# Kernel tuning notes

Hardware: AMD Instinct MI355X
Metric: run time of the kernel (lower is better)

Reference implementation:

```python
import jax, jax.numpy as jnp
import numpy as np

B, LQ, LK = 8, 256, 256
Q_SIZE = K_SIZE = H = D_V = 256
MASK_VALUE = -1000000.0


def setup_inputs() -> dict:
    key = jax.random.key(0)
    kq, kk, kv, kl, kwq, kwk, kwv = jax.random.split(key, 7)
    # Linear weights, torch nn.Linear stores (out, in); init ~ U(-1/sqrt(in), 1/sqrt(in))
    def lin(k, out_f, in_f):
        bound = 1.0 / np.sqrt(in_f)
        return jax.random.uniform(k, (out_f, in_f), jnp.float32, -bound, bound)
    return {
        "queries": jax.random.normal(kq, (B, LQ, Q_SIZE), jnp.float32),
        "keyes": jax.random.normal(kk, (B, LK, K_SIZE), jnp.float32),
        "values": jax.random.normal(kv, (B, LK, D_V), jnp.float32),
        "valid_lens": jax.random.randint(kl, (B,), 1, LK + 1),
        "W_q": lin(kwq, H, Q_SIZE),
        "W_k": lin(kwk, H, K_SIZE),
        "W_v": lin(kwv, 1, H),
    }


def reference(queries, keyes, values, valid_lens, W_q, W_k, W_v):
    # Projections (nn.Linear without bias): x @ W.T
    q = jnp.einsum("bqd,hd->bqh", queries, W_q)            # (B, Lq, H)
    k = jnp.einsum("bkd,hd->bkh", keyes, W_k)              # (B, Lk, H)
    # Broadcast-add + tanh: (B, Lq, Lk, H)
    features = jnp.tanh(q[:, :, None, :] + k[:, None, :, :])
    # W_v reduction H -> 1, squeeze: scores (B, Lq, Lk)
    scores = jnp.einsum("bqkh,h->bqk", features, W_v[0])
    # sequence_mask over the last (key) axis with value -1e6
    lk = scores.shape[-1]
    mask = jnp.arange(lk)[None, None, :] < valid_lens[:, None, None]  # (B,1,Lk)
    scores = jnp.where(mask, scores, MASK_VALUE)
    # NOTE: this repo's masked_softmax normalizes over dim=1 (the query axis),
    # faithfully reproduced here.
    attention_weights = jax.nn.softmax(scores, axis=1)
    # dropout is identity in eval / p=0.0
    return jnp.einsum("bqk,bkd->bqd", attention_weights, values)
```

## Files before the change

### kernel.cpp

```cpp
#include <hip/hip_runtime.h>

typedef float vf4 __attribute__((ext_vector_type(4)));

#define LOG2E 1.4426950408889634f
#define TWO_LOG2E 2.8853900817779268f

__device__ __forceinline__ float fexp2(float x) { return __builtin_amdgcn_exp2f(x); }
__device__ __forceinline__ float frcp(float x) { return __builtin_amdgcn_rcpf(x); }

__global__ __launch_bounds__(256) void proj_kernel(
    const float* __restrict__ queries, const float* __restrict__ keyes,
    const float* __restrict__ Wq, const float* __restrict__ Wk,
    float* __restrict__ Qp, float* __restrict__ Kp) {
  __shared__ alignas(16) float At[16 * 68];
  __shared__ alignas(16) float Bt[16 * 68];
  const int t = threadIdx.x;
  const int m0 = blockIdx.x * 64;
  const int n0 = blockIdx.y * 64;
  const bool isQ = (m0 < 2048);
  const float* X = isQ ? queries : keyes;
  const float* W = isQ ? Wq : Wk;
  float* C = isQ ? Qp : Kp;
  const int mb = isQ ? m0 : (m0 - 2048);

  const int lm = t >> 2;
  const int lq = t & 3;
  const int mm4 = (t & 15) * 4;
  const int nn4 = (t >> 4) * 4;

  float acc[4][4] = {};
  for (int kc = 0; kc < 256; kc += 16) {
    __syncthreads();
    vf4 xa = *(const vf4*)&X[(mb + lm) * 256 + kc + lq * 4];
    vf4 wb = *(const vf4*)&W[(n0 + lm) * 256 + kc + lq * 4];
#pragma unroll
    for (int c = 0; c < 4; ++c) {
      At[(lq * 4 + c) * 68 + lm] = xa[c];
      Bt[(lq * 4 + c) * 68 + lm] = wb[c];
    }
    __syncthreads();
#pragma unroll
    for (int kk = 0; kk < 16; ++kk) {
      vf4 a4 = *(const vf4*)&At[kk * 68 + mm4];
      vf4 b4 = *(const vf4*)&Bt[kk * 68 + nn4];
#pragma unroll
      for (int i = 0; i < 4; ++i)
#pragma unroll
        for (int j = 0; j < 4; ++j) acc[i][j] += a4[i] * b4[j];
    }
  }
#pragma unroll
  for (int i = 0; i < 4; ++i) {
    vf4 o = {acc[i][0] * TWO_LOG2E, acc[i][1] * TWO_LOG2E,
             acc[i][2] * TWO_LOG2E, acc[i][3] * TWO_LOG2E};
    *(vf4*)&C[(mb + mm4 + i) * 256 + n0 + nn4] = o;
  }
}

__global__ __launch_bounds__(256) void scores_exp_kernel(
    const float* __restrict__ Qp, const float* __restrict__ Kp,
    const float* __restrict__ Wv, const int* __restrict__ valid_lens,
    float* __restrict__ E) {
  __shared__ alignas(16) float Qs[32 * 32];
  __shared__ alignas(16) float Ks[32 * 32];
  __shared__ alignas(16) float wvs[256];
  const int t = threadIdx.x;
  const int i0 = blockIdx.x * 32;
  const int j0 = blockIdx.y * 32;
  const int b = blockIdx.z;
  const int ti = t & 15;
  const int tj = t >> 4;

  float Swv;
  {
    vf4 w4 = *(const vf4*)&Wv[(t & 63) * 4];
    float sw = w4[0] + w4[1] + w4[2] + w4[3];
#pragma unroll
    for (int off = 1; off < 64; off <<= 1) sw += __shfl_xor(sw, off, 64);
    Swv = sw;
  }
  if (t < 64) *(vf4*)&wvs[t * 4] = *(const vf4*)&Wv[t * 4];

  const int srow = t >> 3;
  const int scg = t & 7;
  const int swcol = ((scg ^ (srow & 7)) << 2);
  const int qxor = ti & 7;
  const int kxor = tj & 7;

  float acc[2][2] = {};
  for (int hc = 0; hc < 8; ++hc) {
    __syncthreads();
    vf4 qv = *(const vf4*)&Qp[(((b << 8) + i0 + srow) << 8) + hc * 32 + scg * 4];
    vf4 kv = *(const vf4*)&Kp[(((b << 8) + j0 + srow) << 8) + hc * 32 + scg * 4];
    *(vf4*)&Qs[srow * 32 + swcol] = qv;
    *(vf4*)&Ks[srow * 32 + swcol] = kv;
    __syncthreads();
#pragma unroll
    for (int hh = 0; hh < 8; ++hh) {
      vf4 q0 = *(const vf4*)&Qs[ti * 32 + ((hh ^ qxor) << 2)];
      vf4 q1 = *(const vf4*)&Qs[(ti + 16) * 32 + ((hh ^ qxor) << 2)];
      vf4 k0 = *(const vf4*)&Ks[tj * 32 + ((hh ^ kxor) << 2)];
      vf4 k1 = *(const vf4*)&Ks[(tj + 16) * 32 + ((hh ^ kxor) << 2)];
      vf4 wv4 = *(const vf4*)&wvs[hc * 32 + hh * 4];
#pragma unroll
      for (int e = 0; e < 4; ++e) {
        const float we = wv4[e];
        acc[0][0] += we * frcp(fexp2(q0[e] + k0[e]) + 1.0f);
        acc[0][1] += we * frcp(fexp2(q0[e] + k1[e]) + 1.0f);
        acc[1][0] += we * frcp(fexp2(q1[e] + k0[e]) + 1.0f);
        acc[1][1] += we * frcp(fexp2(q1[e] + k1[e]) + 1.0f);
      }
    }
  }

  const int len = valid_lens[b];
#pragma unroll
  for (int c = 0; c < 2; ++c) {
    const int j = j0 + tj + 16 * c;
    const bool masked = (j >= len);
#pragma unroll
    for (int r = 0; r < 2; ++r) {
      const int i = i0 + ti + 16 * r;
      const float score = Swv - 2.0f * acc[r][c];
      const float ev = masked ? 1.0f : fexp2(score * LOG2E);
      E[(((b << 8) + j) << 8) + i] = ev;
    }
  }
}

__global__ __launch_bounds__(256) void rowsum_kernel(
    const float* __restrict__ E, float* __restrict__ R) {
  const int t = threadIdx.x;
  const int l = t & 63;
  const int row = blockIdx.x * 4 + (t >> 6);
  vf4 v = *(const vf4*)&E[(row << 8) + l * 4];
  float s = v[0] + v[1] + v[2] + v[3];
#pragma unroll
  for (int off = 1; off < 64; off <<= 1) s += __shfl_xor(s, off, 64);
  if (l == 0) R[row] = frcp(s);
}

__global__ __launch_bounds__(128) void out_kernel(
    const float* __restrict__ E, const float* __restrict__ R,
    const float* __restrict__ V, float* __restrict__ out) {
  __shared__ alignas(16) float As[32 * 36];
  __shared__ alignas(16) float Bs[32 * 68];
  const int t = threadIdx.x;
  const int i0 = blockIdx.x * 32;
  const int d0 = blockIdx.y * 64;
  const int b = blockIdx.z;
  const int ti = t & 7;
  const int td = t >> 3;
  const int srow = t >> 2;
  const int scg = t & 3;

  float acc[4][4] = {};
  for (int jc = 0; jc < 8; ++jc) {
    const int jb = jc * 32;
    __syncthreads();
    const float rj = R[(b << 8) + jb + srow];
#pragma unroll
    for (int s = 0; s < 2; ++s) {
      const int col = scg * 8 + s * 4;
      vf4 a = *(const vf4*)&E[(((b << 8) + jb + srow) << 8) + i0 + col];
      *(vf4*)&As[srow * 36 + col] = a * rj;
    }
#pragma unroll
    for (int s = 0; s < 4; ++s) {
      const int col = scg * 16 + s * 4;
      *(vf4*)&Bs[srow * 68 + col] =
          *(const vf4*)&V[(((b << 8) + jb + srow) << 8) + d0 + col];
    }
    __syncthreads();
#pragma unroll
    for (int j = 0; j < 32; ++j) {
      vf4 a4 = *(const vf4*)&As[j * 36 + ti * 4];
      vf4 b4 = *(const vf4*)&Bs[j * 68 + td * 4];
#pragma unroll
      for (int r = 0; r < 4; ++r)
#pragma unroll
        for (int c = 0; c < 4; ++c) acc[r][c] += a4[r] * b4[c];
    }
  }
#pragma unroll
  for (int r = 0; r < 4; ++r) {
    vf4 o = {acc[r][0], acc[r][1], acc[r][2], acc[r][3]};
    *(vf4*)&out[(((b << 8) + i0 + ti * 4 + r) << 8) + d0 + td * 4] = o;
  }
}

extern "C" void kernel_launch(void* const* d_in, const int* in_sizes, int n_in,
                              void* d_out, int out_size, void* d_ws, size_t ws_size,
                              hipStream_t stream) {
  const float* queries = (const float*)d_in[0];
  const float* keyes = (const float*)d_in[1];
  const float* values = (const float*)d_in[2];
  const int* valid_lens = (const int*)d_in[3];
  const float* Wq = (const float*)d_in[4];
  const float* Wk = (const float*)d_in[5];
  const float* Wv = (const float*)d_in[6];
  float* out = (float*)d_out;

  float* Qp = (float*)d_ws;
  float* Kp = Qp + 524288;
  float* E = Kp + 524288;
  float* R = E + 524288;

  proj_kernel<<<dim3(64, 4), 256, 0, stream>>>(queries, keyes, Wq, Wk, Qp, Kp);
  scores_exp_kernel<<<dim3(8, 8, 8), 256, 0, stream>>>(Qp, Kp, Wv, valid_lens, E);
  rowsum_kernel<<<512, 256, 0, stream>>>(E, R);
  out_kernel<<<dim3(8, 4, 8), 128, 0, stream>>>(E, R, values, out);
}
```

Measured before the change: 129.7 us.

## Split-K projection and fuse softmax row sums into score kernel via atomics

The projection GEMM is split along K into two halves written to separate buffers, which doubles its block count; the score kernel sums the two halves when it loads them. The separate rowsum kernel is removed. Per-key row sums are reduced with shuffles in the score kernel and accumulated with atomicAdd into a buffer that the projection kernel zeroes. This saves one launch and one full pass over E, at the cost of twice the Q/K projection traffic, extra atomics, and a nondeterministic summation order.

New measurement: 125.4 us. 3.3% less time.

```diff
diff --git a/kernel.cpp b/kernel.cpp
--- a/kernel.cpp
+++ b/kernel.cpp
@@ -11,16 +11,22 @@
 __global__ __launch_bounds__(256) void proj_kernel(
     const float* __restrict__ queries, const float* __restrict__ keyes,
     const float* __restrict__ Wq, const float* __restrict__ Wk,
-    float* __restrict__ Qp, float* __restrict__ Kp) {
+    float* __restrict__ QpH, float* __restrict__ KpH,
+    float* __restrict__ Rsum) {
   __shared__ alignas(16) float At[16 * 68];
   __shared__ alignas(16) float Bt[16 * 68];
   const int t = threadIdx.x;
+  if (blockIdx.x == 0 && blockIdx.y == 0 && blockIdx.z == 0) {
+    *(vf4*)&Rsum[t * 8] = (vf4){0.f, 0.f, 0.f, 0.f};
+    *(vf4*)&Rsum[t * 8 + 4] = (vf4){0.f, 0.f, 0.f, 0.f};
+  }
   const int m0 = blockIdx.x * 64;
   const int n0 = blockIdx.y * 64;
+  const int k0 = blockIdx.z * 128;
   const bool isQ = (m0 < 2048);
   const float* X = isQ ? queries : keyes;
   const float* W = isQ ? Wq : Wk;
-  float* C = isQ ? Qp : Kp;
+  float* C = (isQ ? QpH : KpH) + blockIdx.z * 524288;
   const int mb = isQ ? m0 : (m0 - 2048);
 
   const int lm = t >> 2;
@@ -29,7 +35,7 @@
   const int nn4 = (t >> 4) * 4;
 
   float acc[4][4] = {};
-  for (int kc = 0; kc < 256; kc += 16) {
+  for (int kc = k0; kc < k0 + 128; kc += 16) {
     __syncthreads();
     vf4 xa = *(const vf4*)&X[(mb + lm) * 256 + kc + lq * 4];
     vf4 wb = *(const vf4*)&W[(n0 + lm) * 256 + kc + lq * 4];
@@ -58,9 +64,9 @@
 }
 
 __global__ __launch_bounds__(256) void scores_exp_kernel(
-    const float* __restrict__ Qp, const float* __restrict__ Kp,
+    const float* __restrict__ QpH, const float* __restrict__ KpH,
     const float* __restrict__ Wv, const int* __restrict__ valid_lens,
-    float* __restrict__ E) {
+    float* __restrict__ E, float* __restrict__ Rsum) {
   __shared__ alignas(16) float Qs[32 * 32];
   __shared__ alignas(16) float Ks[32 * 32];
   __shared__ alignas(16) float wvs[256];
@@ -90,10 +96,14 @@
   float acc[2][2] = {};
   for (int hc = 0; hc < 8; ++hc) {
     __syncthreads();
-    vf4 qv = *(const vf4*)&Qp[(((b << 8) + i0 + srow) << 8) + hc * 32 + scg * 4];
-    vf4 kv = *(const vf4*)&Kp[(((b << 8) + j0 + srow) << 8) + hc * 32 + scg * 4];
-    *(vf4*)&Qs[srow * 32 + swcol] = qv;
-    *(vf4*)&Ks[srow * 32 + swcol] = kv;
+    const int qoff = (((b << 8) + i0 + srow) << 8) + hc * 32 + scg * 4;
+    const int koff = (((b << 8) + j0 + srow) << 8) + hc * 32 + scg * 4;
+    vf4 qv = *(const vf4*)&QpH[qoff];
+    vf4 qv2 = *(const vf4*)&QpH[524288 + qoff];
+    vf4 kv = *(const vf4*)&KpH[koff];
+    vf4 kv2 = *(const vf4*)&KpH[524288 + koff];
+    *(vf4*)&Qs[srow * 32 + swcol] = qv + qv2;
+    *(vf4*)&Ks[srow * 32 + swcol] = kv + kv2;
     __syncthreads();
 #pragma unroll
     for (int hh = 0; hh < 8; ++hh) {
@@ -118,30 +128,23 @@
   for (int c = 0; c < 2; ++c) {
     const int j = j0 + tj + 16 * c;
     const bool masked = (j >= len);
+    float ev[2];
 #pragma unroll
     for (int r = 0; r < 2; ++r) {
       const int i = i0 + ti + 16 * r;
       const float score = Swv - 2.0f * acc[r][c];
-      const float ev = masked ? 1.0f : fexp2(score * LOG2E);
-      E[(((b << 8) + j) << 8) + i] = ev;
-    }
-  }
-}
-
-__global__ __launch_bounds__(256) void rowsum_kernel(
-    const float* __restrict__ E, float* __restrict__ R) {
-  const int t = threadIdx.x;
-  const int l = t & 63;
-  const int row = blockIdx.x * 4 + (t >> 6);
-  vf4 v = *(const vf4*)&E[(row << 8) + l * 4];
-  float s = v[0] + v[1] + v[2] + v[3];
-#pragma unroll
-  for (int off = 1; off < 64; off <<= 1) s += __shfl_xor(s, off, 64);
-  if (l == 0) R[row] = frcp(s);
+      ev[r] = masked ? 1.0f : fexp2(score * LOG2E);
+      E[(((b << 8) + j) << 8) + i] = ev[r];
+    }
+    float s = ev[0] + ev[1];
+#pragma unroll
+    for (int off = 1; off < 16; off <<= 1) s += __shfl_xor(s, off, 64);
+    if (ti == 0) atomicAdd(&Rsum[(b << 8) + j], s);
+  }
 }
 
 __global__ __launch_bounds__(128) void out_kernel(
-    const float* __restrict__ E, const float* __restrict__ R,
+    const float* __restrict__ E, const float* __restrict__ Rsum,
     const float* __restrict__ V, float* __restrict__ out) {
   __shared__ alignas(16) float As[32 * 36];
   __shared__ alignas(16) float Bs[32 * 68];
@@ -158,7 +161,7 @@
   for (int jc = 0; jc < 8; ++jc) {
     const int jb = jc * 32;
     __syncthreads();
-    const float rj = R[(b << 8) + jb + srow];
+    const float rj = frcp(Rsum[(b << 8) + jb + srow]);
 #pragma unroll
     for (int s = 0; s < 2; ++s) {
       const int col = scg * 8 + s * 4;
@@ -201,13 +204,14 @@
   const float* Wv = (const float*)d_in[6];
   float* out = (float*)d_out;
 
-  float* Qp = (float*)d_ws;
-  float* Kp = Qp + 524288;
-  float* E = Kp + 524288;
-  float* R = E + 524288;
-
-  proj_kernel<<<dim3(64, 4), 256, 0, stream>>>(queries, keyes, Wq, Wk, Qp, Kp);
-  scores_exp_kernel<<<dim3(8, 8, 8), 256, 0, stream>>>(Qp, Kp, Wv, valid_lens, E);
-  rowsum_kernel<<<512, 256, 0, stream>>>(E, R);
-  out_kernel<<<dim3(8, 4, 8), 128, 0, stream>>>(E, R, values, out);
-}
+  float* QpH = (float*)d_ws;
+  float* KpH = QpH + 2 * 524288;
+  float* E = KpH + 2 * 524288;
+  float* Rsum = E + 524288;
+
+  proj_kernel<<<dim3(64, 4, 2), 256, 0, stream>>>(queries, keyes, Wq, Wk,
+                                                  QpH, KpH, Rsum);
+  scores_exp_kernel<<<dim3(8, 8, 8), 256, 0, stream>>>(QpH, KpH, Wv,
+                                                       valid_lens, E, Rsum);
+  out_kernel<<<dim3(8, 4, 8), 128, 0, stream>>>(E, Rsum, values, out);
+}
```
